# Performance work log

Hardware: AMD Instinct MI355X
Metric: run time of the kernel (lower is better)

Reference implementation:

```python
import jax, jax.numpy as jnp
import numpy as np
import math

INF = 10000000000.0
D_KEY = 64


def setup_inputs() -> dict:
    key = jax.random.key(0)
    kq, kk, kv = jax.random.split(key, 3)
    B, S, D = 4, 4096, D_KEY
    return {
        "query": jax.random.normal(kq, (B, S, D), dtype=jnp.float32),
        "key": jax.random.normal(kk, (B, S, D), dtype=jnp.float32),
        "value": jax.random.normal(kv, (B, S, D), dtype=jnp.float32),
    }


def reference(query, key, value):
    # dot_products: [B, Sq, Sk]
    scale = math.sqrt(D_KEY)
    scores = jnp.einsum("bqd,bkd->bqk", query, key)
    S = key.shape[1]
    # causal: subtract INF on strict upper triangle (triu(1)), before scaling
    tri = jnp.triu(jnp.full((S, S), INF, dtype=scores.dtype), k=1)
    scores = scores - tri[None, :, :]
    logits = scores / scale
    probs = jax.nn.softmax(logits, axis=-1)  # softmax over key dim
    # dropout p=0.0 -> identity
    return jnp.einsum("bqk,bkd->bqd", probs, value)
```

## Files before the change

### kernel.cpp

```cpp
#include <hip/hip_runtime.h>
#include <hip/hip_bf16.h>
#include <math.h>

#define B_  4
#define S_  4096
#define D_  64
#define NQT 64
#define NST 32
#define LDP 68
#define QSC 0.18033688f
#define M0  20.0f

typedef __attribute__((ext_vector_type(8))) short bf16x8;
typedef __attribute__((ext_vector_type(4))) float f32x4;
typedef __attribute__((ext_vector_type(4))) short short4v;

static __device__ inline short f2bf(float f) {
    union { float f; unsigned u; } v; v.f = f;
    unsigned u = v.u;
    unsigned r = u + 0x7fff + ((u >> 16) & 1);
    return (short)(r >> 16);
}
static __device__ inline float bf2f(short s) {
    union { unsigned u; float f; } v; v.u = ((unsigned)(unsigned short)s) << 16;
    return v.f;
}
static __device__ inline unsigned cvt_pk_bf16(float lo, float hi) {
    unsigned r;
    asm("v_cvt_pk_bf16_f32 %0, %1, %2" : "=v"(r) : "v"(lo), "v"(hi));
    return r;
}

__global__ __launch_bounds__(256) void fa_prep(const float* __restrict__ K,
                                               const float* __restrict__ V,
                                               short* __restrict__ Kbf,
                                               short* __restrict__ Vtbf)
{
    const int b   = blockIdx.x >> 6;
    const int st  = blockIdx.x & 63;
    const int tid = threadIdx.x;
    __shared__ short Vs[64 * 72];

    const size_t tbase = ((size_t)b * S_ + (size_t)st * 64) * D_;
    #pragma unroll
    for (int rr = 0; rr < 4; ++rr) {
        int i = tid + rr * 256;
        size_t e = tbase + (size_t)i * 4;
        f32x4 k = *(const f32x4*)(K + e);
        union { short4v s; unsigned u[2]; } ks;
        ks.u[0] = cvt_pk_bf16(k[0], k[1]);
        ks.u[1] = cvt_pk_bf16(k[2], k[3]);
        *(short4v*)(Kbf + e) = ks.s;
        f32x4 v = *(const f32x4*)(V + e);
        int key = i >> 4, d4 = (i & 15) * 4;
        Vs[(d4 + 0) * 72 + key] = f2bf(v[0]);
        Vs[(d4 + 1) * 72 + key] = f2bf(v[1]);
        Vs[(d4 + 2) * 72 + key] = f2bf(v[2]);
        Vs[(d4 + 3) * 72 + key] = f2bf(v[3]);
    }
    __syncthreads();
    #pragma unroll
    for (int cc = 0; cc < 2; ++cc) {
        int c = tid + cc * 256;
        int d = c >> 3, sg = c & 7;
        bf16x8 row = *(const bf16x8*)&Vs[d * 72 + sg * 8];
        *(bf16x8*)(Vtbf + ((size_t)(b * D_ + d)) * S_ + (size_t)st * 64 + sg * 8) = row;
    }
}

__global__ __launch_bounds__(512) void fa_part(const float* __restrict__ Qf,
                                               const short* __restrict__ Kbf,
                                               const short* __restrict__ Vtbf,
                                               short* __restrict__ Opart,
                                               float* __restrict__ Lpart,
                                               int CH, int T)
{
    const int bid = blockIdx.x;
    const int b   = bid / T;
    int r = bid - b * T;
    int qt2 = NST - 1;
    while (true) {
        int n = (2 * qt2 + 2 + CH - 1) / CH;
        if (r < n) break;
        r -= n; --qt2;
    }
    const int kt0 = r * CH;
    const int nkt = 2 * qt2 + 2;
    const int kt1 = (kt0 + CH < nkt) ? kt0 + CH : nkt;

    const int tid  = threadIdx.x;
    const int wave = tid >> 6;
    const int lane = tid & 63;
    const int lm   = lane & 15;
    const int lk   = lane >> 4;

    __shared__ __align__(16) short Ks[64 * 64];
    __shared__ __align__(16) short Vt[64 * 64];
    __shared__ __align__(16) short Ps[128 * LDP];

    bf16x8 qA[2];
    {
        const float* qp = Qf + ((size_t)(b * S_ + qt2 * 128 + wave * 16 + lm)) * D_;
        #pragma unroll
        for (int h = 0; h < 2; ++h) {
            f32x4 a0 = *(const f32x4*)(qp + h * 32 + lk * 8);
            f32x4 a1 = *(const f32x4*)(qp + h * 32 + lk * 8 + 4);
            union { bf16x8 v; unsigned u[4]; } qa;
            qa.u[0] = cvt_pk_bf16(a0[0] * QSC, a0[1] * QSC);
            qa.u[1] = cvt_pk_bf16(a0[2] * QSC, a0[3] * QSC);
            qa.u[2] = cvt_pk_bf16(a1[0] * QSC, a1[1] * QSC);
            qa.u[3] = cvt_pk_bf16(a1[2] * QSC, a1[3] * QSC);
            qA[h] = qa.v;
        }
    }

    bf16x8 onesF;
    #pragma unroll
    for (int j = 0; j < 8; ++j) onesF[j] = (short)0x3F80;

    const int srow = tid >> 3;
    const int sseg = (tid & 7) ^ (srow & 7);
    const char* kgp = (const char*)(Kbf + (size_t)b * S_ * D_)
                    + (size_t)(kt0 * 64 + srow) * 128 + sseg * 16;
    const char* vgp = (const char*)(Vtbf + ((size_t)(b * D_ + srow)) * S_)
                    + (size_t)kt0 * 128 + sseg * 16;

    bf16x8 kreg = *(const bf16x8*)kgp;
    bf16x8 vreg = *(const bf16x8*)vgp;
    kgp += 8192; vgp += 128;

    f32x4 l4 = (f32x4){0.f, 0.f, 0.f, 0.f};
    f32x4 o_acc[4];
    #pragma unroll
    for (int dt = 0; dt < 4; ++dt) o_acc[dt] = (f32x4){0.f, 0.f, 0.f, 0.f};

    const int wrow = wave * 16 + lk * 4;

    for (int kt = kt0; kt < kt1; ++kt) {
        __syncthreads();
        *(bf16x8*)&Ks[tid * 8] = kreg;
        *(bf16x8*)&Vt[tid * 8] = vreg;
        __syncthreads();

        if (kt + 1 < kt1) {
            kreg = *(const bf16x8*)kgp;
            vreg = *(const bf16x8*)vgp;
            kgp += 8192; vgp += 128;
        }

        f32x4 s4[4];
        #pragma unroll
        for (int ct = 0; ct < 4; ++ct) {
            f32x4 acc = (f32x4){-M0, -M0, -M0, -M0};
            #pragma unroll
            for (int h = 0; h < 2; ++h) {
                int seg = (h * 4 + lk) ^ (lm & 7);
                bf16x8 bF = *(const bf16x8*)&Ks[(ct * 16 + lm) * 64 + seg * 8];
                acc = __builtin_amdgcn_mfma_f32_16x16x32_bf16(qA[h], bF, acc, 0, 0, 0);
            }
            s4[ct] = acc;
        }

        if (kt >= 2 * qt2) {
            const int koff = kt * 64 - qt2 * 128;
            #pragma unroll
            for (int ct = 0; ct < 4; ++ct) {
                #pragma unroll
                for (int rr = 0; rr < 4; ++rr) {
                    if (koff + ct * 16 + lm > wrow + rr) s4[ct][rr] = -INFINITY;
                }
            }
        }

        #pragma unroll
        for (int ct = 0; ct < 4; ++ct) {
            #pragma unroll
            for (int rr = 0; rr < 4; ++rr) s4[ct][rr] = exp2f(s4[ct][rr]);
        }
        #pragma unroll
        for (int ct = 0; ct < 4; ++ct) {
            unsigned p01 = cvt_pk_bf16(s4[ct][0], s4[ct][1]);
            unsigned p23 = cvt_pk_bf16(s4[ct][2], s4[ct][3]);
            Ps[(wrow + 0) * LDP + ct * 16 + lm] = (short)(p01 & 0xffff);
            Ps[(wrow + 1) * LDP + ct * 16 + lm] = (short)(p01 >> 16);
            Ps[(wrow + 2) * LDP + ct * 16 + lm] = (short)(p23 & 0xffff);
            Ps[(wrow + 3) * LDP + ct * 16 + lm] = (short)(p23 >> 16);
        }
        bf16x8 aF[2];
        #pragma unroll
        for (int kh = 0; kh < 2; ++kh)
            aF[kh] = *(const bf16x8*)&Ps[(wave * 16 + lm) * LDP + kh * 32 + lk * 8];
        #pragma unroll
        for (int kh = 0; kh < 2; ++kh)
            l4 = __builtin_amdgcn_mfma_f32_16x16x32_bf16(aF[kh], onesF, l4, 0, 0, 0);
        #pragma unroll
        for (int dt = 0; dt < 4; ++dt) {
            #pragma unroll
            for (int kh = 0; kh < 2; ++kh) {
                int seg = (kh * 4 + lk) ^ (lm & 7);
                bf16x8 bF = *(const bf16x8*)&Vt[(dt * 16 + lm) * 64 + seg * 8];
                o_acc[dt] = __builtin_amdgcn_mfma_f32_16x16x32_bf16(aF[kh], bF, o_acc[dt], 0, 0, 0);
            }
        }
    }

    short* Op = Opart + (size_t)bid * (128 * D_);
    if (lm == 0) {
        #pragma unroll
        for (int rr = 0; rr < 4; ++rr)
            Lpart[(size_t)bid * 128 + wrow + rr] = l4[rr];
    }
    #pragma unroll
    for (int dt = 0; dt < 4; ++dt) {
        unsigned o01 = cvt_pk_bf16(o_acc[dt][0], o_acc[dt][1]);
        unsigned o23 = cvt_pk_bf16(o_acc[dt][2], o_acc[dt][3]);
        Op[(wrow + 0) * D_ + dt * 16 + lm] = (short)(o01 & 0xffff);
        Op[(wrow + 1) * D_ + dt * 16 + lm] = (short)(o01 >> 16);
        Op[(wrow + 2) * D_ + dt * 16 + lm] = (short)(o23 & 0xffff);
        Op[(wrow + 3) * D_ + dt * 16 + lm] = (short)(o23 >> 16);
    }
}

__global__ __launch_bounds__(256) void fa_combine(const short* __restrict__ Opart,
                                                  const float* __restrict__ Lpart,
                                                  float* __restrict__ O,
                                                  int CH, int T)
{
    const int idx = blockIdx.x * 256 + threadIdx.x;
    const int b   = idx / (S_ * 16);
    const int rem = idx - b * (S_ * 16);
    const int q   = rem >> 4;
    const int d4  = (rem & 15) << 2;
    const int qt2 = q >> 7;
    const int rit = q & 127;

    int F = 0;
    for (int y = qt2 + 1; y < NST; ++y) F += (2 * y + 2 + CH - 1) / CH;
    const int base = b * T + F;
    const int nch  = (2 * qt2 + 2 + CH - 1) / CH;

    float L = 0.f;
    f32x4 acc = (f32x4){0.f, 0.f, 0.f, 0.f};
    for (int c = 0; c < nch; ++c) {
        L += Lpart[(size_t)(base + c) * 128 + rit];
        short4v o = *(const short4v*)(Opart + (size_t)(base + c) * (128 * D_) + rit * D_ + d4);
        acc[0] += bf2f(o[0]); acc[1] += bf2f(o[1]);
        acc[2] += bf2f(o[2]); acc[3] += bf2f(o[3]);
    }
    float inv = 1.f / L;
    f32x4 outv;
    outv[0] = acc[0] * inv; outv[1] = acc[1] * inv;
    outv[2] = acc[2] * inv; outv[3] = acc[3] * inv;
    *(f32x4*)(O + (size_t)idx * 4) = outv;
}

__global__ __launch_bounds__(256) void fa_fwd(const float* __restrict__ Q,
                                              const float* __restrict__ K,
                                              const float* __restrict__ V,
                                              float* __restrict__ O)
{
    const int qt   = (gridDim.x - 1) - blockIdx.x;
    const int b    = blockIdx.y;
    const int tid  = threadIdx.x;
    const int wave = tid >> 6;
    const int lane = tid & 63;
    const int lm   = lane & 15;
    const int lk   = lane >> 4;

    __shared__ short Ks[64 * 72];
    __shared__ short Vt[64 * 72];
    __shared__ short Ps[64 * 72];

    const float* Qb = Q + ((size_t)b * S_ + (size_t)qt * 64) * D_;
    const float* Kb = K + (size_t)b * S_ * D_;
    const float* Vb = V + (size_t)b * S_ * D_;

    bf16x8 qA[2];
    {
        const float* qp = Qb + (wave * 16 + lm) * D_;
        #pragma unroll
        for (int h = 0; h < 2; ++h) {
            const float* p = qp + h * 32 + lk * 8;
            #pragma unroll
            for (int j = 0; j < 8; ++j) qA[h][j] = f2bf(p[j] * 0.125f);
        }
    }
    float m_i[4], l_i[4];
    f32x4 o_acc[4];
    #pragma unroll
    for (int rr = 0; rr < 4; ++rr) { m_i[rr] = -INFINITY; l_i[rr] = 0.f; }
    #pragma unroll
    for (int dt = 0; dt < 4; ++dt) o_acc[dt] = (f32x4){0.f, 0.f, 0.f, 0.f};

    const int n_kt = qt + 1;
    for (int kt = 0; kt < n_kt; ++kt) {
        __syncthreads();
        #pragma unroll
        for (int rr = 0; rr < 4; ++rr) {
            int i   = tid + rr * 256;
            int row = i >> 4;
            int c4  = (i & 15) * 4;
            const size_t gbase = ((size_t)(kt * 64 + row)) * D_ + c4;
            f32x4 kv = *(const f32x4*)(Kb + gbase);
            short4v ks;
            ks[0] = f2bf(kv[0]); ks[1] = f2bf(kv[1]);
            ks[2] = f2bf(kv[2]); ks[3] = f2bf(kv[3]);
            *(short4v*)&Ks[row * 72 + c4] = ks;
            f32x4 vv = *(const f32x4*)(Vb + gbase);
            Vt[(c4 + 0) * 72 + row] = f2bf(vv[0]);
            Vt[(c4 + 1) * 72 + row] = f2bf(vv[1]);
            Vt[(c4 + 2) * 72 + row] = f2bf(vv[2]);
            Vt[(c4 + 3) * 72 + row] = f2bf(vv[3]);
        }
        __syncthreads();
        f32x4 s4[4];
        #pragma unroll
        for (int ct = 0; ct < 4; ++ct) {
            f32x4 acc = (f32x4){0.f, 0.f, 0.f, 0.f};
            #pragma unroll
            for (int h = 0; h < 2; ++h) {
                bf16x8 bF = *(const bf16x8*)&Ks[(ct * 16 + lm) * 72 + h * 32 + lk * 8];
                acc = __builtin_amdgcn_mfma_f32_16x16x32_bf16(qA[h], bF, acc, 0, 0, 0);
            }
            s4[ct] = acc;
        }
        if (kt == qt) {
            #pragma unroll
            for (int ct = 0; ct < 4; ++ct) {
                #pragma unroll
                for (int rr = 0; rr < 4; ++rr) {
                    int qrow = wave * 16 + lk * 4 + rr;
                    int kcol = ct * 16 + lm;
                    if (kcol > qrow) s4[ct][rr] = -INFINITY;
                }
            }
        }
        float alpha[4];
        #pragma unroll
        for (int rr = 0; rr < 4; ++rr) {
            float mx = fmaxf(fmaxf(s4[0][rr], s4[1][rr]), fmaxf(s4[2][rr], s4[3][rr]));
            mx = fmaxf(mx, __shfl_xor(mx, 1));
            mx = fmaxf(mx, __shfl_xor(mx, 2));
            mx = fmaxf(mx, __shfl_xor(mx, 4));
            mx = fmaxf(mx, __shfl_xor(mx, 8));
            float mn = fmaxf(m_i[rr], mx);
            alpha[rr] = __expf(m_i[rr] - mn);
            m_i[rr] = mn;
        }
        float rsum[4] = {0.f, 0.f, 0.f, 0.f};
        #pragma unroll
        for (int ct = 0; ct < 4; ++ct) {
            #pragma unroll
            for (int rr = 0; rr < 4; ++rr) {
                float p = __expf(s4[ct][rr] - m_i[rr]);
                s4[ct][rr] = p;
                rsum[rr] += p;
            }
        }
        #pragma unroll
        for (int rr = 0; rr < 4; ++rr) {
            float rs = rsum[rr];
            rs += __shfl_xor(rs, 1);
            rs += __shfl_xor(rs, 2);
            rs += __shfl_xor(rs, 4);
            rs += __shfl_xor(rs, 8);
            l_i[rr] = l_i[rr] * alpha[rr] + rs;
        }
        #pragma unroll
        for (int ct = 0; ct < 4; ++ct) {
            #pragma unroll
            for (int rr = 0; rr < 4; ++rr) {
                Ps[(wave * 16 + lk * 4 + rr) * 72 + ct * 16 + lm] = f2bf(s4[ct][rr]);
            }
        }
        #pragma unroll
        for (int dt = 0; dt < 4; ++dt) {
            #pragma unroll
            for (int rr = 0; rr < 4; ++rr) o_acc[dt][rr] *= alpha[rr];
        }
        #pragma unroll
        for (int dt = 0; dt < 4; ++dt) {
            #pragma unroll
            for (int kh = 0; kh < 2; ++kh) {
                bf16x8 aF = *(const bf16x8*)&Ps[(wave * 16 + lm) * 72 + kh * 32 + lk * 8];
                bf16x8 bF = *(const bf16x8*)&Vt[(dt * 16 + lm) * 72 + kh * 32 + lk * 8];
                o_acc[dt] = __builtin_amdgcn_mfma_f32_16x16x32_bf16(aF, bF, o_acc[dt], 0, 0, 0);
            }
        }
    }
    float* Ob = O + ((size_t)b * S_ + (size_t)qt * 64) * D_;
    #pragma unroll
    for (int rr = 0; rr < 4; ++rr) {
        float inv = 1.f / l_i[rr];
        int row = wave * 16 + lk * 4 + rr;
        #pragma unroll
        for (int dt = 0; dt < 4; ++dt) {
            Ob[row * D_ + dt * 16 + lm] = o_acc[dt][rr] * inv;
        }
    }
}

extern "C" void kernel_launch(void* const* d_in, const int* in_sizes, int n_in,
                              void* d_out, int out_size, void* d_ws, size_t ws_size,
                              hipStream_t stream) {
    const float* Q = (const float*)d_in[0];
    const float* K = (const float*)d_in[1];
    const float* V = (const float*)d_in[2];
    float* O = (float*)d_out;

    const size_t convShorts = (size_t)B_ * S_ * D_;
    int CH = 0, T = 0;
    const int chs[5] = {4, 8, 16, 32, 64};
    for (int k = 0; k < 5; ++k) {
        int c = chs[k];
        int t = 0;
        for (int q2 = 0; q2 < NST; ++q2) t += (2 * q2 + 2 + c - 1) / c;
        size_t need = 2 * convShorts * 2
                    + (size_t)B_ * t * (128 * D_) * 2
                    + (size_t)B_ * t * 128 * 4;
        if (need <= ws_size) { CH = c; T = t; break; }
    }
    if (CH == 0) {
        dim3 grid(NQT, B_);
        fa_fwd<<<grid, 256, 0, stream>>>(Q, K, V, O);
        return;
    }
    short* Kbf   = (short*)d_ws;
    short* Vtbf  = Kbf + convShorts;
    short* Opart = Vtbf + convShorts;
    float* Lpart = (float*)(Opart + (size_t)B_ * T * (128 * D_));

    fa_prep<<<dim3(B_ * NQT), 256, 0, stream>>>(K, V, Kbf, Vtbf);
    fa_part<<<dim3(B_ * T), 512, 0, stream>>>(Q, Kbf, Vtbf, Opart, Lpart, CH, T);
    fa_combine<<<dim3((B_ * S_ * 16) / 256), 256, 0, stream>>>(Opart, Lpart, O, CH, T);
}
```

Baseline: 99.89 us.

## Load K and V MFMA fragments directly from global memory, dropping LDS staging

Removes the shared-memory staging of K and transposed V tiles, along with the two block-wide barriers and the register prefetch per key tile. Each wave now reads its MFMA B-operand fragments straight from global memory (through the caches). This trades barrier and LDS-write overhead for redundant global/L2 traffic, since every wave now fetches the same K/V data. It also loses the software prefetch that overlapped the next tile's load with compute.

```diff
diff --git a/kernel.cpp b/kernel.cpp
--- a/kernel.cpp
+++ b/kernel.cpp
@@ -94,8 +94,6 @@
     const int lm   = lane & 15;
     const int lk   = lane >> 4;
 
-    __shared__ __align__(16) short Ks[64 * 64];
-    __shared__ __align__(16) short Vt[64 * 64];
     __shared__ __align__(16) short Ps[128 * LDP];
 
     bf16x8 qA[2];
@@ -118,16 +116,13 @@
     #pragma unroll
     for (int j = 0; j < 8; ++j) onesF[j] = (short)0x3F80;
 
-    const int srow = tid >> 3;
-    const int sseg = (tid & 7) ^ (srow & 7);
-    const char* kgp = (const char*)(Kbf + (size_t)b * S_ * D_)
-                    + (size_t)(kt0 * 64 + srow) * 128 + sseg * 16;
-    const char* vgp = (const char*)(Vtbf + ((size_t)(b * D_ + srow)) * S_)
-                    + (size_t)kt0 * 128 + sseg * 16;
-
-    bf16x8 kreg = *(const bf16x8*)kgp;
-    bf16x8 vreg = *(const bf16x8*)vgp;
-    kgp += 8192; vgp += 128;
+    const short* Kb = Kbf + (size_t)b * S_ * D_;
+    const short* Vb = Vtbf + (size_t)b * D_ * S_;
+    const short* kRow = Kb + (size_t)lm * D_ + lk * 8;
+    const short* vRow[4];
+    #pragma unroll
+    for (int dt = 0; dt < 4; ++dt)
+        vRow[dt] = Vb + (size_t)(dt * 16 + lm) * S_ + lk * 8;
 
     f32x4 l4 = (f32x4){0.f, 0.f, 0.f, 0.f};
     f32x4 o_acc[4];
@@ -137,25 +132,13 @@
     const int wrow = wave * 16 + lk * 4;
 
     for (int kt = kt0; kt < kt1; ++kt) {
-        __syncthreads();
-        *(bf16x8*)&Ks[tid * 8] = kreg;
-        *(bf16x8*)&Vt[tid * 8] = vreg;
-        __syncthreads();
-
-        if (kt + 1 < kt1) {
-            kreg = *(const bf16x8*)kgp;
-            vreg = *(const bf16x8*)vgp;
-            kgp += 8192; vgp += 128;
-        }
-
         f32x4 s4[4];
         #pragma unroll
         for (int ct = 0; ct < 4; ++ct) {
             f32x4 acc = (f32x4){-M0, -M0, -M0, -M0};
             #pragma unroll
             for (int h = 0; h < 2; ++h) {
-                int seg = (h * 4 + lk) ^ (lm & 7);
-                bf16x8 bF = *(const bf16x8*)&Ks[(ct * 16 + lm) * 64 + seg * 8];
+                bf16x8 bF = *(const bf16x8*)(kRow + (size_t)(kt * 64 + ct * 16) * D_ + h * 32);
                 acc = __builtin_amdgcn_mfma_f32_16x16x32_bf16(qA[h], bF, acc, 0, 0, 0);
             }
             s4[ct] = acc;
@@ -197,8 +180,7 @@
         for (int dt = 0; dt < 4; ++dt) {
             #pragma unroll
             for (int kh = 0; kh < 2; ++kh) {
-                int seg = (kh * 4 + lk) ^ (lm & 7);
-                bf16x8 bF = *(const bf16x8*)&Vt[(dt * 16 + lm) * 64 + seg * 8];
+                bf16x8 bF = *(const bf16x8*)(vRow[dt] + (size_t)kt * 64 + kh * 32);
                 o_acc[dt] = __builtin_amdgcn_mfma_f32_16x16x32_bf16(aF[kh], bF, o_acc[dt], 0, 0, 0);
             }
         }
```

After: 155.4 us. 1.56x slower.
